# Kernel optimization log

Measured on AMD Instinct MI355X. Metric: run time of the kernel, lower is better.

## Reference

```python
import jax, jax.numpy as jnp
import numpy as np

EPS = 1e-5
DN = ('NCHW', 'OIHW', 'NCHW')

def _conv(x, w):
    return jax.lax.conv_general_dilated(x, w, (1, 1), 'VALID', dimension_numbers=DN)

def _bn4(x, g, b, m, v):
    # BatchNorm2d in eval mode, per-channel over NCHW
    inv = g / jnp.sqrt(v + EPS)
    return x * inv[None, :, None, None] + (b - m * inv)[None, :, None, None]

def _bn1(x, g, b, m, v):
    inv = g / jnp.sqrt(v + EPS)
    return x * inv[None, :] + (b - m * inv)[None, :]

def _hardtanh(x):
    return jnp.clip(x, -1.0, 1.0)

def _sign(x):
    return jnp.sign(x)

def _maxpool2(x):
    return jax.lax.reduce_window(x, -jnp.inf, jax.lax.max,
                                 (1, 1, 2, 2), (1, 1, 2, 2), 'VALID')

def setup_inputs() -> dict:
    key = jax.random.key(0)
    ks = jax.random.split(key, 20)
    B = 8192
    d = {
        'x': jax.random.normal(ks[0], (B, 8, 16, 16), jnp.float32),
        'w0': jax.random.normal(ks[1], (32, 8, 3, 3), jnp.float32) * 0.1,
        'b0': jax.random.normal(ks[2], (32,), jnp.float32) * 0.1,
        'g1': jax.random.uniform(ks[3], (32,), jnp.float32, 0.5, 1.5),
        'be1': jax.random.normal(ks[4], (32,), jnp.float32) * 0.1,
        'm1': jax.random.normal(ks[5], (32,), jnp.float32) * 0.1,
        'v1': jax.random.uniform(ks[6], (32,), jnp.float32, 0.5, 1.5),
        'w2': jax.random.normal(ks[7], (32, 32, 3, 3), jnp.float32) * 0.1,
        'g2': jax.random.uniform(ks[8], (32,), jnp.float32, 0.5, 1.5),
        'be2': jax.random.normal(ks[9], (32,), jnp.float32) * 0.1,
        'm2': jax.random.normal(ks[10], (32,), jnp.float32) * 0.1,
        'v2': jax.random.uniform(ks[11], (32,), jnp.float32, 0.5, 1.5),
        'w_fc': jax.random.normal(ks[12], (516, 1152), jnp.float32) * 0.03,
        'g3': jax.random.uniform(ks[13], (516,), jnp.float32, 0.5, 1.5),
        'be3': jax.random.normal(ks[14], (516,), jnp.float32) * 0.1,
        'm3': jax.random.normal(ks[15], (516,), jnp.float32) * 0.1,
        'v3': jax.random.uniform(ks[16], (516,), jnp.float32, 0.5, 1.5),
        'w_last': jax.random.normal(ks[17], (10, 516), jnp.float32) * 0.05,
        'b_last': jax.random.normal(ks[18], (10,), jnp.float32) * 0.05,
    }
    return d

def reference(x, w0, b0, g1, be1, m1, v1, w2, g2, be2, m2, v2,
              w_fc, g3, be3, m3, v3, w_last, b_last):
    # initial float conv + BN + Hardtanh
    h = _conv(x, w0) + b0[None, :, None, None]          # [B,32,14,14]
    h = _hardtanh(_bn4(h, g1, be1, m1, v1))
    # binarized conv (sign(input), sign(weight), no bias)
    h = _conv(_sign(h), _sign(w2))                      # [B,32,12,12]
    h = _hardtanh(_bn4(h, g2, be2, m2, v2))
    h = _maxpool2(h)                                    # [B,32,6,6]
    # dropout is identity in eval mode
    h = h.reshape(h.shape[0], -1)                       # [B,1152]
    # binarized linear (no bias)
    h = _sign(h) @ _sign(w_fc).T                        # [B,516]
    h = _hardtanh(_bn1(h, g3, be3, m3, v3))
    return h @ w_last.T + b_last[None, :]               # [B,10]
```

## Files before the change

kernel.cpp:

```cpp
#include <hip/hip_runtime.h>
#include <cstdint>

#define EPSF 1e-5f

typedef __attribute__((ext_vector_type(8))) short short8;
typedef __attribute__((ext_vector_type(4))) float f32x4;
typedef __attribute__((ext_vector_type(4))) unsigned int u32x4;

__device__ inline uint32_t bf16rne(float x) {
    uint32_t u = __builtin_bit_cast(uint32_t, x);
    return (u + 0x7fffu + ((u >> 16) & 1u)) >> 16;
}
__device__ inline float bf16f(uint32_t b) {
    return __builtin_bit_cast(float, b << 16);
}

__global__ __launch_bounds__(256) void prep_kernel(
    const float* __restrict__ w2, const float* __restrict__ wfc,
    const float* __restrict__ g3, const float* __restrict__ be3,
    const float* __restrict__ m3, const float* __restrict__ v3,
    const float* __restrict__ wlast,
    const float* __restrict__ w0, const float* __restrict__ b0,
    const float* __restrict__ g1, const float* __restrict__ be1,
    const float* __restrict__ m1, const float* __restrict__ v1,
    uint32_t* __restrict__ w2bits, uint32_t* __restrict__ wfcb,
    float* __restrict__ inv3p, float* __restrict__ sh3p, float* __restrict__ wlt,
    uint32_t* __restrict__ bfrag, float2* __restrict__ bn1c)
{
    int id = blockIdx.x * 256 + threadIdx.x;
    if (id < 288) {
        int co = id / 9, r = id % 9;
        uint32_t b = 0;
        for (int ci = 0; ci < 32; ci++)
            b |= (uint32_t)(w2[(co * 32 + ci) * 9 + r] < 0.f) << ci;
        w2bits[id] = b;
        return;
    }
    id -= 288;
    if (id < 36 * 576) {
        int j = id / 36, pos = id % 36;
        uint32_t b = 0;
        if (j < 516) {
            const float* row = wfc + j * 1152 + pos;
            for (int c = 0; c < 32; c++)
                b |= (uint32_t)(row[c * 36] < 0.f) << c;
        }
        wfcb[pos * 576 + j] = b;
        return;
    }
    id -= 36 * 576;
    if (id < 576) {
        float iv = 0.f, sh = 0.f;
        if (id < 516) {
            iv = g3[id] / sqrtf(__fadd_rn(v3[id], EPSF));
            sh = __fsub_rn(be3[id], __fmul_rn(m3[id], iv));
        }
        inv3p[id] = iv; sh3p[id] = sh;
        return;
    }
    id -= 576;
    if (id < 5760) {
        int k = id / 576, j = id % 576;
        wlt[id] = (j < 516) ? wlast[k * 516 + j] : 0.f;
        return;
    }
    id -= 5760;
    if (id < 768) {
        int L = id / 12, r = id % 12;
        int nt = r / 6, s = (r % 6) / 2, h = r & 1;
        int g = L >> 4, n = L & 15;
        int tap = 4 * s + g;
        uint32_t d[4] = {0, 0, 0, 0};
        if (tap < 9) {
            int co = nt * 16 + n;
            for (int j2 = 0; j2 < 4; j2++) {
                float wa = w0[co * 72 + (2 * j2) * 9 + tap];
                float wb = w0[co * 72 + (2 * j2 + 1) * 9 + tap];
                uint32_t ha = bf16rne(wa), hb = bf16rne(wb);
                uint32_t va, vb;
                if (h == 0) { va = ha; vb = hb; }
                else { va = bf16rne(wa - bf16f(ha)); vb = bf16rne(wb - bf16f(hb)); }
                d[j2] = va | (vb << 16);
            }
        }
        *(u32x4*)(bfrag + id * 4) = (u32x4){d[0], d[1], d[2], d[3]};
        return;
    }
    id -= 768;
    if (id < 32) {
        float iv = g1[id] / sqrtf(__fadd_rn(v1[id], EPSF));
        float sh = __fsub_rn(be1[id], __fmul_rn(m1[id], iv));
        float off = __fadd_rn(__fmul_rn(b0[id], iv), sh);
        bn1c[id] = make_float2(iv, off);
    }
}

__device__ __noinline__ bool recheck_sign(const float* __restrict__ xim,
                                          const float* __restrict__ w0,
                                          int py, int px, int co,
                                          float ivc, float offc)
{
    double ad = 0.0;
    for (int ci = 0; ci < 8; ci++)
        for (int ky = 0; ky < 3; ky++)
            for (int kx = 0; kx < 3; kx++)
                ad = fma((double)xim[ci * 256 + (py + ky) * 16 + px + kx],
                         (double)w0[co * 72 + ci * 9 + ky * 3 + kx], ad);
    return (ad * (double)ivc + (double)offc) < 0.0;
}

__global__ __launch_bounds__(128, 4) void convA(
    const float* __restrict__ x, const float* __restrict__ w0,
    const uint32_t* __restrict__ bfrag, const float2* __restrict__ bn1c,
    uint32_t* __restrict__ s1bits)
{
    __shared__ __align__(16) char simg[2][9216];

    const int t = threadIdx.x;
    const int wv = t >> 6, lane = t & 63;
    const int img = blockIdx.x * 2 + wv;
    const float* xim = x + img * 2048;
    char* hib = simg[wv];
    char* lob = simg[wv] + 4608;

    const int g = lane >> 4;
    const int n = lane & 15;

    short8 Bh[2][3], Bl[2][3];
    {
        const uint32_t* bb = bfrag + lane * 48;
        #pragma unroll
        for (int nt = 0; nt < 2; nt++)
            #pragma unroll
            for (int s = 0; s < 3; s++) {
                Bh[nt][s] = *(const short8*)(bb + (nt * 6 + s * 2) * 4);
                Bl[nt][s] = *(const short8*)(bb + (nt * 6 + s * 2 + 1) * 4);
            }
    }
    const float2 bnA = bn1c[n], bnB = bn1c[16 + n];

    #pragma unroll
    for (int q = 0; q < 4; q++) {
        int pos = lane + 64 * q;
        uint32_t hw[4], lw[4];
        #pragma unroll
        for (int j2 = 0; j2 < 4; j2++) {
            float a = xim[(2 * j2) * 256 + pos];
            float b = xim[(2 * j2 + 1) * 256 + pos];
            uint32_t ha = bf16rne(a), hb = bf16rne(b);
            uint32_t la = bf16rne(a - bf16f(ha)), lb = bf16rne(b - bf16f(hb));
            hw[j2] = ha | (hb << 16);
            lw[j2] = la | (lb << 16);
        }
        *(u32x4*)(hib + pos * 16) = (u32x4){hw[0], hw[1], hw[2], hw[3]};
        *(u32x4*)(lob + pos * 16) = (u32x4){lw[0], lw[1], lw[2], lw[3]};
    }
    if (lane < 32) {
        *(u32x4*)(hib + (256 + lane) * 16) = (u32x4){0, 0, 0, 0};
        *(u32x4*)(lob + (256 + lane) * 16) = (u32x4){0, 0, 0, 0};
    }

    int koff[3];
    #pragma unroll
    for (int s = 0; s < 3; s++) {
        int tap = 4 * s + g;
        koff[s] = (tap < 9) ? ((tap / 3) * 16 + (tap % 3)) * 16 : 0;
    }

    __syncthreads();

    uint32_t* outb = s1bits + img * 196;

    for (int tile = 0; tile < 13; ++tile) {
        int posA = tile * 16 + n;
        int pyA = posA / 14, pxA = posA - pyA * 14;
        int sl = (pyA * 16 + pxA) * 16;

        f32x4 acc0 = {0.f, 0.f, 0.f, 0.f}, acc1 = {0.f, 0.f, 0.f, 0.f};
        #pragma unroll
        for (int s = 0; s < 3; s++) {
            short8 Ah = *(const short8*)(hib + sl + koff[s]);
            short8 Al = *(const short8*)(lob + sl + koff[s]);
            acc0 = __builtin_amdgcn_mfma_f32_16x16x32_bf16(Al, Bh[0][s], acc0, 0, 0, 0);
            acc0 = __builtin_amdgcn_mfma_f32_16x16x32_bf16(Ah, Bl[0][s], acc0, 0, 0, 0);
            acc0 = __builtin_amdgcn_mfma_f32_16x16x32_bf16(Ah, Bh[0][s], acc0, 0, 0, 0);
            acc1 = __builtin_amdgcn_mfma_f32_16x16x32_bf16(Al, Bh[1][s], acc1, 0, 0, 0);
            acc1 = __builtin_amdgcn_mfma_f32_16x16x32_bf16(Ah, Bl[1][s], acc1, 0, 0, 0);
            acc1 = __builtin_amdgcn_mfma_f32_16x16x32_bf16(Ah, Bh[1][s], acc1, 0, 0, 0);
        }

        #pragma unroll
        for (int r = 0; r < 4; r++) {
            int pos = tile * 16 + 4 * g + r;
            float yv0 = fmaf(acc0[r], bnA.x, bnA.y);
            float yv1 = fmaf(acc1[r], bnB.x, bnB.y);
            bool bit0, bit1;
            if (__builtin_expect(pos < 196 && fabsf(yv0) < 3e-4f, 0)) {
                int py = pos / 14, px = pos - py * 14;
                bit0 = recheck_sign(xim, w0, py, px, n, bnA.x, bnA.y);
            } else bit0 = (yv0 < 0.f);
            if (__builtin_expect(pos < 196 && fabsf(yv1) < 3e-4f, 0)) {
                int py = pos / 14, px = pos - py * 14;
                bit1 = recheck_sign(xim, w0, py, px, 16 + n, bnB.x, bnB.y);
            } else bit1 = (yv1 < 0.f);
            unsigned long long m0 = __ballot(bit0);
            unsigned long long m1 = __ballot(bit1);
            uint32_t word = (uint32_t)((m0 >> (16 * g)) & 0xffffull)
                          | ((uint32_t)((m1 >> (16 * g)) & 0xffffull) << 16);
            if (n == 0 && pos < 196) outb[pos] = word;
        }
    }
}

__global__ __launch_bounds__(256) void convB(
    const uint32_t* __restrict__ s1bits, const uint32_t* __restrict__ w2bits,
    const float* __restrict__ g2, const float* __restrict__ be2,
    const float* __restrict__ m2, const float* __restrict__ v2,
    uint32_t* __restrict__ fcin)
{
    __shared__ uint32_t s1l[4][196];
    const int t = threadIdx.x, wid = t >> 6, lane = t & 63;
    const int img = blockIdx.x * 4 + wid;

    for (int i = lane; i < 196; i += 64) s1l[wid][i] = s1bits[img * 196 + i];

    const int c = lane & 31, h = lane >> 5;
    uint32_t wr[9];
    #pragma unroll
    for (int k = 0; k < 9; k++) wr[k] = w2bits[c * 9 + k];
    float ivv = g2[c] / sqrtf(__fadd_rn(v2[c], EPSF));
    float shv = __fsub_rn(be2[c], __fmul_rn(m2[c], ivv));
    __syncthreads();

    const uint32_t* s1w = s1l[wid];
    uint32_t* outp = fcin + img * 36;

    for (int yy = 0; yy < 3; yy++) {
        const int y2 = yy + 3 * h;
        const int rbase = 2 * y2 * 14;
        uint32_t win[4][4];
        #pragma unroll
        for (int rr = 0; rr < 4; rr++) {
            uint2 a = *(const uint2*)&s1w[rbase + rr * 14];
            uint2 b = *(const uint2*)&s1w[rbase + rr * 14 + 2];
            win[rr][0] = a.x; win[rr][1] = a.y; win[rr][2] = b.x; win[rr][3] = b.y;
        }
        for (int x2 = 0; x2 < 6; x2++) {
            if (x2 > 0) {
                #pragma unroll
                for (int rr = 0; rr < 4; rr++) {
                    win[rr][0] = win[rr][2]; win[rr][1] = win[rr][3];
                    uint2 b = *(const uint2*)&s1w[rbase + rr * 14 + 2 * x2 + 2];
                    win[rr][2] = b.x; win[rr][3] = b.y;
                }
            }
            int mx = -10000;
            #pragma unroll
            for (int dy = 0; dy < 2; dy++)
                #pragma unroll
                for (int dx = 0; dx < 2; dx++) {
                    int p = 0;
                    #pragma unroll
                    for (int ky = 0; ky < 3; ky++)
                        #pragma unroll
                        for (int kx = 0; kx < 3; kx++)
                            p += __popc(win[dy + ky][dx + kx] ^ wr[ky * 3 + kx]);
                    mx = max(mx, 288 - 2 * p);
                }
            float yv = __fadd_rn(__fmul_rn((float)mx, ivv), shv);
            unsigned long long mb = __ballot(yv < 0.f);
            int pos = y2 * 6 + x2;
            if (lane == 0)  outp[pos] = (uint32_t)mb;
            if (lane == 32) outp[pos] = (uint32_t)(mb >> 32);
        }
    }
}

__global__ __launch_bounds__(256) void fcC(
    const uint32_t* __restrict__ fcin, const uint32_t* __restrict__ wfcb,
    const float* __restrict__ inv3p, const float* __restrict__ sh3p,
    const float* __restrict__ wlt, const float* __restrict__ blast,
    float* __restrict__ out)
{
    __shared__ uint32_t l_in[288];
    const int t = threadIdx.x, wid = t >> 6, lane = t & 63;

    for (int i = t; i < 288; i += 256) l_in[i] = fcin[blockIdx.x * 288 + i];
    __syncthreads();

    const int b0i = blockIdx.x * 8 + wid * 2;
    const uint32_t* in0 = &l_in[wid * 72];

    int pc0[9], pc1[9];
    #pragma unroll
    for (int q = 0; q < 9; q++) { pc0[q] = 0; pc1[q] = 0; }

    for (int w = 0; w < 36; w++) {
        uint32_t i0 = in0[w], i1 = in0[36 + w];
        const uint32_t* wf = wfcb + w * 576 + lane;
        #pragma unroll
        for (int q = 0; q < 9; q++) {
            uint32_t f = wf[q * 64];
            pc0[q] += __popc(i0 ^ f);
            pc1[q] += __popc(i1 ^ f);
        }
    }

    float oa[2][10];
    #pragma unroll
    for (int b = 0; b < 2; b++)
        #pragma unroll
        for (int k = 0; k < 10; k++) oa[b][k] = 0.f;

    #pragma unroll
    for (int q = 0; q < 9; q++) {
        int j = lane + 64 * q;
        float ivv = inv3p[j], shv = sh3p[j];
        float t0 = fminf(1.f, fmaxf(-1.f, __fadd_rn(__fmul_rn((float)(1152 - 2 * pc0[q]), ivv), shv)));
        float t1 = fminf(1.f, fmaxf(-1.f, __fadd_rn(__fmul_rn((float)(1152 - 2 * pc1[q]), ivv), shv)));
        #pragma unroll
        for (int k = 0; k < 10; k++) {
            float wv = wlt[k * 576 + j];
            oa[0][k] = fmaf(t0, wv, oa[0][k]);
            oa[1][k] = fmaf(t1, wv, oa[1][k]);
        }
    }

    #pragma unroll
    for (int m = 1; m < 64; m <<= 1)
        #pragma unroll
        for (int b = 0; b < 2; b++)
            #pragma unroll
            for (int k = 0; k < 10; k++)
                oa[b][k] += __shfl_xor(oa[b][k], m, 64);

    if (lane == 0) {
        for (int b = 0; b < 2; b++)
            for (int k = 0; k < 10; k++)
                out[(b0i + b) * 10 + k] = oa[b][k] + blast[k];
    }
}

extern "C" void kernel_launch(void* const* d_in, const int* in_sizes, int n_in,
                              void* d_out, int out_size, void* d_ws, size_t ws_size,
                              hipStream_t stream)
{
    (void)in_sizes; (void)n_in; (void)out_size; (void)ws_size;
    const float* x     = (const float*)d_in[0];
    const float* w0    = (const float*)d_in[1];
    const float* b0    = (const float*)d_in[2];
    const float* g1    = (const float*)d_in[3];
    const float* be1   = (const float*)d_in[4];
    const float* m1    = (const float*)d_in[5];
    const float* v1    = (const float*)d_in[6];
    const float* w2    = (const float*)d_in[7];
    const float* g2    = (const float*)d_in[8];
    const float* be2   = (const float*)d_in[9];
    const float* m2    = (const float*)d_in[10];
    const float* v2    = (const float*)d_in[11];
    const float* wfc   = (const float*)d_in[12];
    const float* g3    = (const float*)d_in[13];
    const float* be3   = (const float*)d_in[14];
    const float* m3    = (const float*)d_in[15];
    const float* v3    = (const float*)d_in[16];
    const float* wlast = (const float*)d_in[17];
    const float* blast = (const float*)d_in[18];

    char* ws = (char*)d_ws;
    uint32_t* s1bits = (uint32_t*)(ws);
    uint32_t* fcin   = (uint32_t*)(ws + 6422528);
    uint32_t* w2bits = (uint32_t*)(ws + 7602176);
    uint32_t* wfcb   = (uint32_t*)(ws + 7603328);
    float*    inv3p  = (float*)(ws + 7686272);
    float*    sh3p   = (float*)(ws + 7688576);
    float*    wlt    = (float*)(ws + 7690880);
    uint32_t* bfrag  = (uint32_t*)(ws + 7713920);
    float2*   bn1c   = (float2*)(ws + 7726208);

    prep_kernel<<<110, 256, 0, stream>>>(w2, wfc, g3, be3, m3, v3, wlast,
                                         w0, b0, g1, be1, m1, v1,
                                         w2bits, wfcb, inv3p, sh3p, wlt,
                                         bfrag, bn1c);
    convA<<<4096, 128, 0, stream>>>(x, w0, bfrag, bn1c, s1bits);
    convB<<<2048, 256, 0, stream>>>(s1bits, w2bits, g2, be2, m2, v2, fcin);
    fcC<<<1024, 256, 0, stream>>>(fcin, wfcb, inv3p, sh3p, wlt, blast, (float*)d_out);
}
```

Before: 225.0 us.

## Fuse binary conv and FC kernels, split convA tiles across wave pairs, ballot-pack FC weights

Merges the binarized conv/maxpool kernel with the FC kernel so the packed FC input bits stay in LDS instead of going through global memory, and removes one launch. convA now runs two waves per image, which split the staging loads and the 13 MFMA tiles to raise parallelism per block. Prep packs FC weight signs with a wave ballot instead of a 32-iteration strided loop per thread. The fused kernel runs each wave over two images serially before the FC stage, which can lengthen the per-block critical path.

```diff
diff --git a/kernel.cpp b/kernel.cpp
--- a/kernel.cpp
+++ b/kernel.cpp
@@ -27,7 +27,23 @@
     float* __restrict__ inv3p, float* __restrict__ sh3p, float* __restrict__ wlt,
     uint32_t* __restrict__ bfrag, float2* __restrict__ bn1c)
 {
-    int id = blockIdx.x * 256 + threadIdx.x;
+    const int tid = threadIdx.x;
+    if (blockIdx.x < 129) {
+        const int wid = tid >> 6, lane = tid & 63;
+        const int j = blockIdx.x * 4 + wid;
+        const int c = lane & 31, pp = lane >> 5;
+        const float* row = wfc + j * 1152 + c * 36;
+        #pragma unroll
+        for (int i = 0; i < 18; i++) {
+            int pos = 2 * i + pp;
+            float v = row[pos];
+            unsigned long long mb = __ballot(v < 0.f);
+            if (lane == 0)  wfcb[(2 * i) * 576 + j]     = (uint32_t)mb;
+            if (lane == 32) wfcb[(2 * i + 1) * 576 + j] = (uint32_t)(mb >> 32);
+        }
+        return;
+    }
+    int id = (blockIdx.x - 129) * 256 + tid;
     if (id < 288) {
         int co = id / 9, r = id % 9;
         uint32_t b = 0;
@@ -37,18 +53,6 @@
         return;
     }
     id -= 288;
-    if (id < 36 * 576) {
-        int j = id / 36, pos = id % 36;
-        uint32_t b = 0;
-        if (j < 516) {
-            const float* row = wfc + j * 1152 + pos;
-            for (int c = 0; c < 32; c++)
-                b |= (uint32_t)(row[c * 36] < 0.f) << c;
-        }
-        wfcb[pos * 576 + j] = b;
-        return;
-    }
-    id -= 36 * 576;
     if (id < 576) {
         float iv = 0.f, sh = 0.f;
         if (id < 516) {
@@ -92,6 +96,12 @@
         float sh = __fsub_rn(be1[id], __fmul_rn(m1[id], iv));
         float off = __fadd_rn(__fmul_rn(b0[id], iv), sh);
         bn1c[id] = make_float2(iv, off);
+        return;
+    }
+    id -= 32;
+    if (id < 2160) {
+        int p = id / 60, j = 516 + id % 60;
+        wfcb[p * 576 + j] = 0u;
     }
 }
 
@@ -109,7 +119,7 @@
     return (ad * (double)ivc + (double)offc) < 0.0;
 }
 
-__global__ __launch_bounds__(128, 4) void convA(
+__global__ __launch_bounds__(256, 4) void convA(
     const float* __restrict__ x, const float* __restrict__ w0,
     const uint32_t* __restrict__ bfrag, const float2* __restrict__ bn1c,
     uint32_t* __restrict__ s1bits)
@@ -118,10 +128,12 @@
 
     const int t = threadIdx.x;
     const int wv = t >> 6, lane = t & 63;
-    const int img = blockIdx.x * 2 + wv;
+    const int ilocal = wv >> 1;
+    const int w01 = wv & 1;
+    const int img = blockIdx.x * 2 + ilocal;
     const float* xim = x + img * 2048;
-    char* hib = simg[wv];
-    char* lob = simg[wv] + 4608;
+    char* hib = simg[ilocal];
+    char* lob = simg[ilocal] + 4608;
 
     const int g = lane >> 4;
     const int n = lane & 15;
@@ -140,13 +152,15 @@
     const float2 bnA = bn1c[n], bnB = bn1c[16 + n];
 
     #pragma unroll
-    for (int q = 0; q < 4; q++) {
-        int pos = lane + 64 * q;
+    for (int q = 0; q < 2; q++) {
+        int pos = w01 * 128 + 64 * q + lane;
+        float v[8];
+        #pragma unroll
+        for (int ci = 0; ci < 8; ci++) v[ci] = xim[ci * 256 + pos];
         uint32_t hw[4], lw[4];
         #pragma unroll
         for (int j2 = 0; j2 < 4; j2++) {
-            float a = xim[(2 * j2) * 256 + pos];
-            float b = xim[(2 * j2 + 1) * 256 + pos];
+            float a = v[2 * j2], b = v[2 * j2 + 1];
             uint32_t ha = bf16rne(a), hb = bf16rne(b);
             uint32_t la = bf16rne(a - bf16f(ha)), lb = bf16rne(b - bf16f(hb));
             hw[j2] = ha | (hb << 16);
@@ -155,7 +169,7 @@
         *(u32x4*)(hib + pos * 16) = (u32x4){hw[0], hw[1], hw[2], hw[3]};
         *(u32x4*)(lob + pos * 16) = (u32x4){lw[0], lw[1], lw[2], lw[3]};
     }
-    if (lane < 32) {
+    if (w01 == 1 && lane < 32) {
         *(u32x4*)(hib + (256 + lane) * 16) = (u32x4){0, 0, 0, 0};
         *(u32x4*)(lob + (256 + lane) * 16) = (u32x4){0, 0, 0, 0};
     }
@@ -170,8 +184,9 @@
     __syncthreads();
 
     uint32_t* outb = s1bits + img * 196;
-
-    for (int tile = 0; tile < 13; ++tile) {
+    const int tstart = w01 ? 7 : 0, tend = w01 ? 13 : 7;
+
+    for (int tile = tstart; tile < tend; ++tile) {
         int posA = tile * 16 + n;
         int pyA = posA / 14, pxA = posA - pyA * 14;
         int sl = (pyA * 16 + pxA) * 16;
@@ -212,17 +227,21 @@
     }
 }
 
-__global__ __launch_bounds__(256) void convB(
+__global__ __launch_bounds__(256) void convBF(
     const uint32_t* __restrict__ s1bits, const uint32_t* __restrict__ w2bits,
     const float* __restrict__ g2, const float* __restrict__ be2,
     const float* __restrict__ m2, const float* __restrict__ v2,
-    uint32_t* __restrict__ fcin)
-{
-    __shared__ uint32_t s1l[4][196];
+    const uint32_t* __restrict__ wfcb,
+    const float* __restrict__ inv3p, const float* __restrict__ sh3p,
+    const float* __restrict__ wlt, const float* __restrict__ blast,
+    float* __restrict__ out)
+{
+    __shared__ uint32_t s1l[8][196];
+    __shared__ uint32_t l_in[288];
     const int t = threadIdx.x, wid = t >> 6, lane = t & 63;
-    const int img = blockIdx.x * 4 + wid;
-
-    for (int i = lane; i < 196; i += 64) s1l[wid][i] = s1bits[img * 196 + i];
+
+    for (int i = t; i < 1568; i += 256)
+        ((uint32_t*)s1l)[i] = s1bits[blockIdx.x * 1568 + i];
 
     const int c = lane & 31, h = lane >> 5;
     uint32_t wr[9];
@@ -232,60 +251,51 @@
     float shv = __fsub_rn(be2[c], __fmul_rn(m2[c], ivv));
     __syncthreads();
 
-    const uint32_t* s1w = s1l[wid];
-    uint32_t* outp = fcin + img * 36;
-
-    for (int yy = 0; yy < 3; yy++) {
-        const int y2 = yy + 3 * h;
-        const int rbase = 2 * y2 * 14;
-        uint32_t win[4][4];
-        #pragma unroll
-        for (int rr = 0; rr < 4; rr++) {
-            uint2 a = *(const uint2*)&s1w[rbase + rr * 14];
-            uint2 b = *(const uint2*)&s1w[rbase + rr * 14 + 2];
-            win[rr][0] = a.x; win[rr][1] = a.y; win[rr][2] = b.x; win[rr][3] = b.y;
-        }
-        for (int x2 = 0; x2 < 6; x2++) {
-            if (x2 > 0) {
+    for (int rep = 0; rep < 2; rep++) {
+        const int iml = wid * 2 + rep;
+        const uint32_t* s1w = s1l[iml];
+        uint32_t* outp = &l_in[iml * 36];
+
+        for (int yy = 0; yy < 3; yy++) {
+            const int y2 = yy + 3 * h;
+            const int rbase = 2 * y2 * 14;
+            uint32_t win[4][4];
+            #pragma unroll
+            for (int rr = 0; rr < 4; rr++) {
+                uint2 a = *(const uint2*)&s1w[rbase + rr * 14];
+                uint2 b = *(const uint2*)&s1w[rbase + rr * 14 + 2];
+                win[rr][0] = a.x; win[rr][1] = a.y; win[rr][2] = b.x; win[rr][3] = b.y;
+            }
+            for (int x2 = 0; x2 < 6; x2++) {
+                if (x2 > 0) {
+                    #pragma unroll
+                    for (int rr = 0; rr < 4; rr++) {
+                        win[rr][0] = win[rr][2]; win[rr][1] = win[rr][3];
+                        uint2 b = *(const uint2*)&s1w[rbase + rr * 14 + 2 * x2 + 2];
+                        win[rr][2] = b.x; win[rr][3] = b.y;
+                    }
+                }
+                int mx = -10000;
                 #pragma unroll
-                for (int rr = 0; rr < 4; rr++) {
-                    win[rr][0] = win[rr][2]; win[rr][1] = win[rr][3];
-                    uint2 b = *(const uint2*)&s1w[rbase + rr * 14 + 2 * x2 + 2];
-                    win[rr][2] = b.x; win[rr][3] = b.y;
-                }
+                for (int dy = 0; dy < 2; dy++)
+                    #pragma unroll
+                    for (int dx = 0; dx < 2; dx++) {
+                        int p = 0;
+                        #pragma unroll
+                        for (int ky = 0; ky < 3; ky++)
+                            #pragma unroll
+                            for (int kx = 0; kx < 3; kx++)
+                                p += __popc(win[dy + ky][dx + kx] ^ wr[ky * 3 + kx]);
+                        mx = max(mx, 288 - 2 * p);
+                    }
+                float yv = __fadd_rn(__fmul_rn((float)mx, ivv), shv);
+                unsigned long long mb = __ballot(yv < 0.f);
+                int pos = y2 * 6 + x2;
+                if (lane == 0)  outp[pos] = (uint32_t)mb;
+                if (lane == 32) outp[pos] = (uint32_t)(mb >> 32);
             }
-            int mx = -10000;
-            #pragma unroll
-            for (int dy = 0; dy < 2; dy++)
-                #pragma unroll
-                for (int dx = 0; dx < 2; dx++) {
-                    int p = 0;
-                    #pragma unroll
-                    for (int ky = 0; ky < 3; ky++)
-                        #pragma unroll
-                        for (int kx = 0; kx < 3; kx++)
-                            p += __popc(win[dy + ky][dx + kx] ^ wr[ky * 3 + kx]);
-                    mx = max(mx, 288 - 2 * p);
-                }
-            float yv = __fadd_rn(__fmul_rn((float)mx, ivv), shv);
-            unsigned long long mb = __ballot(yv < 0.f);
-            int pos = y2 * 6 + x2;
-            if (lane == 0)  outp[pos] = (uint32_t)mb;
-            if (lane == 32) outp[pos] = (uint32_t)(mb >> 32);
-        }
-    }
-}
-
-__global__ __launch_bounds__(256) void fcC(
-    const uint32_t* __restrict__ fcin, const uint32_t* __restrict__ wfcb,
-    const float* __restrict__ inv3p, const float* __restrict__ sh3p,
-    const float* __restrict__ wlt, const float* __restrict__ blast,
-    float* __restrict__ out)
-{
-    __shared__ uint32_t l_in[288];
-    const int t = threadIdx.x, wid = t >> 6, lane = t & 63;
-
-    for (int i = t; i < 288; i += 256) l_in[i] = fcin[blockIdx.x * 288 + i];
+        }
+    }
     __syncthreads();
 
     const int b0i = blockIdx.x * 8 + wid * 2;
@@ -315,14 +325,14 @@
     #pragma unroll
     for (int q = 0; q < 9; q++) {
         int j = lane + 64 * q;
-        float ivv = inv3p[j], shv = sh3p[j];
-        float t0 = fminf(1.f, fmaxf(-1.f, __fadd_rn(__fmul_rn((float)(1152 - 2 * pc0[q]), ivv), shv)));
-        float t1 = fminf(1.f, fmaxf(-1.f, __fadd_rn(__fmul_rn((float)(1152 - 2 * pc1[q]), ivv), shv)));
+        float iv3 = inv3p[j], sh3 = sh3p[j];
+        float t0 = fminf(1.f, fmaxf(-1.f, __fadd_rn(__fmul_rn((float)(1152 - 2 * pc0[q]), iv3), sh3)));
+        float t1 = fminf(1.f, fmaxf(-1.f, __fadd_rn(__fmul_rn((float)(1152 - 2 * pc1[q]), iv3), sh3)));
         #pragma unroll
         for (int k = 0; k < 10; k++) {
-            float wv = wlt[k * 576 + j];
-            oa[0][k] = fmaf(t0, wv, oa[0][k]);
-            oa[1][k] = fmaf(t1, wv, oa[1][k]);
+            float wvv = wlt[k * 576 + j];
+            oa[0][k] = fmaf(t0, wvv, oa[0][k]);
+            oa[1][k] = fmaf(t1, wvv, oa[1][k]);
         }
     }
 
@@ -368,20 +378,19 @@
 
     char* ws = (char*)d_ws;
     uint32_t* s1bits = (uint32_t*)(ws);
-    uint32_t* fcin   = (uint32_t*)(ws + 6422528);
-    uint32_t* w2bits = (uint32_t*)(ws + 7602176);
-    uint32_t* wfcb   = (uint32_t*)(ws + 7603328);
-    float*    inv3p  = (float*)(ws + 7686272);
-    float*    sh3p   = (float*)(ws + 7688576);
-    float*    wlt    = (float*)(ws + 7690880);
-    uint32_t* bfrag  = (uint32_t*)(ws + 7713920);
-    float2*   bn1c   = (float2*)(ws + 7726208);
-
-    prep_kernel<<<110, 256, 0, stream>>>(w2, wfc, g3, be3, m3, v3, wlast,
+    uint32_t* w2bits = (uint32_t*)(ws + 6422528);
+    uint32_t* wfcb   = (uint32_t*)(ws + 6423680);
+    float*    inv3p  = (float*)(ws + 6506624);
+    float*    sh3p   = (float*)(ws + 6508928);
+    float*    wlt    = (float*)(ws + 6511232);
+    uint32_t* bfrag  = (uint32_t*)(ws + 6534272);
+    float2*   bn1c   = (float2*)(ws + 6546560);
+
+    prep_kernel<<<167, 256, 0, stream>>>(w2, wfc, g3, be3, m3, v3, wlast,
                                          w0, b0, g1, be1, m1, v1,
                                          w2bits, wfcb, inv3p, sh3p, wlt,
                                          bfrag, bn1c);
-    convA<<<4096, 128, 0, stream>>>(x, w0, bfrag, bn1c, s1bits);
-    convB<<<2048, 256, 0, stream>>>(s1bits, w2bits, g2, be2, m2, v2, fcin);
-    fcC<<<1024, 256, 0, stream>>>(fcin, wfcb, inv3p, sh3p, wlt, blast, (float*)d_out);
-}
+    convA<<<4096, 256, 0, stream>>>(x, w0, bfrag, bn1c, s1bits);
+    convBF<<<1024, 256, 0, stream>>>(s1bits, w2bits, g2, be2, m2, v2,
+                                     wfcb, inv3p, sh3p, wlt, blast, (float*)d_out);
+}
```

New measurement: 226.6 us. Within noise of the previous version (+0.7%).
